# Kernel optimization log

Hardware: AMD Instinct MI355X
Metric: run time of the kernel (lower is better)

The kernel has to match this reference:

```python
import jax, jax.numpy as jnp
import numpy as np
import math

L, D, H = 4, 256, 8
HD = D // H
B, SQ, SK = 2, 1024, 1024
FF = 3 * D
EPS = 1e-5


def setup_inputs() -> dict:
    key = jax.random.key(0)
    ks = jax.random.split(key, 16)
    s = 0.02
    w = lambda k, shape: jax.random.normal(k, shape, jnp.float32) * s
    return {
        "pose": jax.random.normal(ks[0], (B, SQ, D), jnp.float32),
        "vel": jax.random.normal(ks[1], (B, SK, D), jnp.float32),
        "img": jax.random.normal(ks[2], (B, SK, D), jnp.float32),
        "Wq": w(ks[3], (L, D, D)), "bq": jnp.zeros((L, D), jnp.float32),
        "Wk": w(ks[4], (L, D, D)), "bk": jnp.zeros((L, D), jnp.float32),
        "Wv": w(ks[5], (L, D, D)), "bv": jnp.zeros((L, D), jnp.float32),
        "Wo": w(ks[6], (L, D, D)), "bo": jnp.zeros((L, D), jnp.float32),
        "an_g": jnp.ones((L, D), jnp.float32), "an_b": jnp.zeros((L, D), jnp.float32),
        "W1": w(ks[7], (L, D, FF)), "b1": jnp.zeros((L, FF), jnp.float32),
        "W2": w(ks[8], (L, FF, D)), "b2": jnp.zeros((L, D), jnp.float32),
        "fn_g": jnp.ones((L, D), jnp.float32), "fn_b": jnp.zeros((L, D), jnp.float32),
        "n_g": jnp.ones((L, D), jnp.float32), "n_b": jnp.zeros((L, D), jnp.float32),
    }


def entmax15(x):
    # exact alpha=1.5 entmax along the last axis (Peters & Martins 2019)
    x = x * 0.5
    x = x - jnp.max(x, axis=-1, keepdims=True)
    z = -jnp.sort(-x, axis=-1)  # descending
    k = jnp.arange(1, z.shape[-1] + 1, dtype=x.dtype)
    mean = jnp.cumsum(z, axis=-1) / k
    mean_sq = jnp.cumsum(z * z, axis=-1) / k
    ss = k * (mean_sq - mean * mean)
    delta = jnp.clip((1.0 - ss) / k, 0.0)
    tau = mean - jnp.sqrt(delta)
    support = jnp.sum(tau <= z, axis=-1, keepdims=True)  # support size >= 1
    tau_star = jnp.take_along_axis(tau, support - 1, axis=-1)
    p = jnp.clip(x - tau_star, 0.0)
    return p * p


def layer_norm(x, g, b):
    m = jnp.mean(x, axis=-1, keepdims=True)
    v = jnp.mean((x - m) ** 2, axis=-1, keepdims=True)
    return (x - m) * jax.lax.rsqrt(v + EPS) * g + b


def mish(x):
    return x * jnp.tanh(jax.nn.softplus(x))


def reference(pose, vel, img, Wq, bq, Wk, bk, Wv, bv, Wo, bo, an_g, an_b,
              W1, b1, W2, b2, fn_g, fn_b, n_g, n_b):
    def mha(q_in, kv, i):
        bs, sq, _ = q_in.shape
        sk = kv.shape[1]
        q = (q_in @ Wq[i] + bq[i]).reshape(bs, sq, H, HD)
        k = (kv @ Wk[i] + bk[i]).reshape(bs, sk, H, HD)
        v = (kv @ Wv[i] + bv[i]).reshape(bs, sk, H, HD)
        scores = jnp.einsum('bqhd,bkhd->bhqk', q, k) / math.sqrt(HD)
        attn = entmax15(scores)
        out = jnp.einsum('bhqk,bkhd->bqhd', attn, v).reshape(bs, sq, D)
        return out @ Wo[i] + bo[i]

    def cross_layer(x1, x2, i):
        y = layer_norm(mha(x1, x2, i), an_g[i], an_b[i])
        x1 = x1 + y
        y = layer_norm(x1, fn_g[i], fn_b[i])
        h = mish(y @ W1[i] + b1[i]) @ W2[i] + b2[i]
        return x1 + h

    def stack(x, kv):
        for i in range(L):  # small fixed layer loop (shared weights across both paths)
            mem = x
            x = cross_layer(x, kv, i)
            x = layer_norm(x, n_g[i], n_b[i])
            x = x + mem
        return x

    img_out = stack(pose, img)
    pose_out = stack(pose, vel)
    return (pose_out, img_out)
```

## Files before the change

kernel.cpp:

```cpp
#include <hip/hip_runtime.h>
#include <math.h>

#define NL   4
#define DIM  256
#define NH   8
#define HDIM 32
#define SQL  1024
#define SKL  1024
#define FFD  768
#define CB   4
#define ROWS (CB * SQL)

typedef __attribute__((ext_vector_type(8))) short bf16x8;
typedef __attribute__((ext_vector_type(4))) short bf16x4;
typedef __attribute__((ext_vector_type(4))) float f32x4;
typedef __attribute__((ext_vector_type(2))) float f32x2;


__device__ __forceinline__ short f2bf(float f) {
    union { float f; unsigned u; } v; v.f = f;
    unsigned u = v.u + 0x7fffu + ((v.u >> 16) & 1u);
    return (short)(u >> 16);
}

__device__ __forceinline__ float fast_mish(float x) {
    float u = __expf(fminf(x, 20.0f));
    float a = __builtin_fmaf(u, u, 2.0f * u);
    return x * a * __builtin_amdgcn_rcpf(a + 2.0f);
}

__device__ __forceinline__ f32x2 lo2(f32x4 v) { return __builtin_shufflevector(v, v, 0, 1); }
__device__ __forceinline__ f32x2 hi2(f32x4 v) { return __builtin_shufflevector(v, v, 2, 3); }


__global__ __launch_bounds__(256) void init_kernel(
        const float* __restrict__ pose, const float* __restrict__ vel,
        const float* __restrict__ img, float* __restrict__ X,
        short* __restrict__ Xb, short* __restrict__ KVb) {
    int idx = blockIdx.x * 256 + threadIdx.x;
    if (idx >= CB * SQL * DIM) return;
    int c = idx / (SQL * DIM);
    int rem = idx - c * (SQL * DIM);
    int b = c & 1;
    float pv = pose[b * SQL * DIM + rem];
    X[idx]  = pv;
    Xb[idx] = f2bf(pv);
    const float* kv = (c < 2) ? vel : img;
    KVb[idx] = f2bf(kv[b * SQL * DIM + rem]);
}


__global__ __launch_bounds__(256) void transpose_qkvo(
        const float* __restrict__ Wq, const float* __restrict__ Wk,
        const float* __restrict__ Wv, const float* __restrict__ Wo,
        short* __restrict__ Wqt, short* __restrict__ Wkt,
        short* __restrict__ Wvt, short* __restrict__ Wot) {
    __shared__ float tile[64][65];
    int z = blockIdx.z, m = z >> 2, lyr = z & 3;
    const float* src = ((m == 0) ? Wq : (m == 1) ? Wk : (m == 2) ? Wv : Wo)
                       + (size_t)lyr * DIM * DIM;
    short* dst = ((m == 0) ? Wqt : (m == 1) ? Wkt : (m == 2) ? Wvt : Wot)
                 + (size_t)lyr * DIM * DIM;
    int t = threadIdx.x;
    int n0 = blockIdx.x * 64, k0 = blockIdx.y * 64;
#pragma unroll
    for (int i = 0; i < 16; i++) {
        int idx = t + i * 256;
        int r = idx >> 6, c = idx & 63;
        tile[r][c] = src[(size_t)(k0 + r) * DIM + n0 + c];
    }
    __syncthreads();
#pragma unroll
    for (int i = 0; i < 16; i++) {
        int idx = t + i * 256;
        int r = idx >> 6, c = idx & 63;
        dst[(size_t)(n0 + r) * DIM + k0 + c] = f2bf(tile[c][r]);
    }
}

__global__ __launch_bounds__(256) void transpose_w(
        const float* __restrict__ src, short* __restrict__ dst, int K, int N) {
    __shared__ float tile[64][65];
    int t = threadIdx.x;
    int n0 = blockIdx.x * 64, k0 = blockIdx.y * 64;
    const float* s = src + (size_t)blockIdx.z * K * N;
    short* d = dst + (size_t)blockIdx.z * K * N;
#pragma unroll
    for (int i = 0; i < 16; i++) {
        int idx = t + i * 256;
        int r = idx >> 6, c = idx & 63;
        tile[r][c] = s[(size_t)(k0 + r) * N + n0 + c];
    }
    __syncthreads();
#pragma unroll
    for (int i = 0; i < 16; i++) {
        int idx = t + i * 256;
        int r = idx >> 6, c = idx & 63;
        d[(size_t)(n0 + r) * K + k0 + c] = f2bf(tile[c][r]);
    }
}


__global__ __launch_bounds__(256) void qkv_gemm(
        const short* __restrict__ Xb, const short* __restrict__ KVb,
        const short* __restrict__ Wqt, const short* __restrict__ Wkt,
        const short* __restrict__ Wvt,
        const float* __restrict__ bq, const float* __restrict__ bk,
        const float* __restrict__ bv,
        short* __restrict__ Qb, short* __restrict__ Kb, short* __restrict__ Vt,
        float qscale) {
    int z = blockIdx.z;
    const short* A    = (z == 0) ? Xb : KVb;
    const short* Wt   = (z == 0) ? Wqt : (z == 1) ? Wkt : Wvt;
    const float* bias = (z == 0) ? bq : (z == 1) ? bk : bv;
    float scale = (z == 0) ? qscale : 1.0f;

    int t = threadIdx.x, l = t & 63, w = t >> 6;
    int lq = l & 15, lg = l >> 4;
    int bm = blockIdx.y * 64, bn = blockIdx.x * 64;

    const short* ap = A + (size_t)(bm + w * 16 + lq) * DIM + lg * 8;
    const short* wp = Wt + (size_t)(bn + lq) * DIM + lg * 8;

    f32x4 acc[4];
#pragma unroll
    for (int nt = 0; nt < 4; nt++) acc[nt] = (f32x4){0.f, 0.f, 0.f, 0.f};
#pragma unroll
    for (int k0 = 0; k0 < DIM; k0 += 32) {
        bf16x8 af = *(const bf16x8*)(ap + k0);
#pragma unroll
        for (int nt = 0; nt < 4; nt++) {
            bf16x8 bfr = *(const bf16x8*)(wp + (size_t)nt * 16 * DIM + k0);
            acc[nt] = __builtin_amdgcn_mfma_f32_16x16x32_bf16(af, bfr, acc[nt], 0, 0, 0);
        }
    }

    int ms = bm + w * 16 + lg * 4;
#pragma unroll
    for (int nt = 0; nt < 4; nt++) {
        int col = bn + nt * 16 + lq;
        float bv_ = bias[col];
        float v[4];
#pragma unroll
        for (int j = 0; j < 4; j++) v[j] = acc[nt][j] + bv_;
        if (z < 2) {
            short* out = (z == 0) ? Qb : Kb;
#pragma unroll
            for (int j = 0; j < 4; j++) out[(size_t)(ms + j) * DIM + col] = f2bf(v[j] * scale);
        } else {
            int cc = ms >> 10, kl = ms & 1023;
            bf16x4 pk;
#pragma unroll
            for (int j = 0; j < 4; j++) pk[j] = f2bf(v[j]);
            *(bf16x4*)(Vt + ((size_t)(cc * DIM + col)) * SKL + kl) = pk;
        }
    }
}


__global__ __launch_bounds__(256) void gemm_ln2(
        const short* __restrict__ A, const short* __restrict__ Wt,
        const float* __restrict__ bias, const float* __restrict__ Xres,
        const float* __restrict__ ag, const float* __restrict__ ab,
        const float* __restrict__ fg, const float* __restrict__ fb,
        float* __restrict__ x1out, short* __restrict__ yout) {
    __shared__ float gbuf[16][264];
    int t = threadIdx.x, l = t & 63, w = t >> 6;
    int lq = l & 15, lg = l >> 4;
    int bm = blockIdx.x * 16;

    const short* ap = A + (size_t)(bm + lq) * DIM + lg * 8;
    const short* wp = Wt + (size_t)(w * 64 + lq) * DIM + lg * 8;

    f32x4 acc[4];
#pragma unroll
    for (int nt = 0; nt < 4; nt++) acc[nt] = (f32x4){0.f, 0.f, 0.f, 0.f};
#pragma unroll
    for (int k0 = 0; k0 < DIM; k0 += 32) {
        bf16x8 af = *(const bf16x8*)(ap + k0);
#pragma unroll
        for (int nt = 0; nt < 4; nt++) {
            bf16x8 bfr = *(const bf16x8*)(wp + (size_t)nt * 16 * DIM + k0);
            acc[nt] = __builtin_amdgcn_mfma_f32_16x16x32_bf16(af, bfr, acc[nt], 0, 0, 0);
        }
    }
#pragma unroll
    for (int nt = 0; nt < 4; nt++) {
        int col = w * 64 + nt * 16 + lq;
        float bv_ = bias[col];
#pragma unroll
        for (int j = 0; j < 4; j++) gbuf[lg * 4 + j][col] = acc[nt][j] + bv_;
    }
    __syncthreads();

    int g = t >> 4, u = t & 15;
    int row = bm + g;
    float s = 0.f, s2 = 0.f;
#pragma unroll
    for (int i = 0; i < 16; i++) {
        float v = gbuf[g][u + 16 * i];
        s += v; s2 += v * v;
    }
#pragma unroll
    for (int off = 1; off < 16; off <<= 1) { s += __shfl_xor(s, off); s2 += __shfl_xor(s2, off); }
    float m = s * (1.f / DIM);
    float rstd = rsqrtf(s2 * (1.f / DIM) - m * m + 1e-5f);

    float x1v[16];
    float sb = 0.f, sb2 = 0.f;
#pragma unroll
    for (int i = 0; i < 16; i++) {
        int col = u + 16 * i;
        float x1 = Xres[(size_t)row * DIM + col] + (gbuf[g][col] - m) * rstd * ag[col] + ab[col];
        x1v[i] = x1; sb += x1; sb2 += x1 * x1;
    }
#pragma unroll
    for (int off = 1; off < 16; off <<= 1) { sb += __shfl_xor(sb, off); sb2 += __shfl_xor(sb2, off); }
    float m2 = sb * (1.f / DIM);
    float rstd2 = rsqrtf(sb2 * (1.f / DIM) - m2 * m2 + 1e-5f);
#pragma unroll
    for (int i = 0; i < 16; i++) {
        int col = u + 16 * i;
        x1out[(size_t)row * DIM + col] = x1v[i];
        yout[(size_t)row * DIM + col]  = f2bf((x1v[i] - m2) * rstd2 * fg[col] + fb[col]);
    }
}


__global__ __launch_bounds__(256) void gemm_ffn(
        const short* __restrict__ Yb, const short* __restrict__ W1t,
        const float* __restrict__ b1, const short* __restrict__ W2t,
        const float* __restrict__ b2, const float* __restrict__ x1res,
        const float* __restrict__ Xres, const float* __restrict__ g_,
        const float* __restrict__ b_,
        float* __restrict__ outf, short* __restrict__ outb) {
    __shared__ __align__(16) char lds[16 * 776 * 2];
    short (*g1)[776]  = (short(*)[776])lds;
    float (*gbuf)[264] = (float(*)[264])lds;

    int t = threadIdx.x, l = t & 63, w = t >> 6;
    int lq = l & 15, lg = l >> 4;
    int bm = blockIdx.x * 16;

    {
        const short* ap = Yb + (size_t)(bm + lq) * DIM + lg * 8;
        const short* wp = W1t + (size_t)(w * 192 + lq) * DIM + lg * 8;
        f32x4 acc[12];
#pragma unroll
        for (int nt = 0; nt < 12; nt++) acc[nt] = (f32x4){0.f, 0.f, 0.f, 0.f};
#pragma unroll
        for (int k0 = 0; k0 < DIM; k0 += 32) {
            bf16x8 af = *(const bf16x8*)(ap + k0);
#pragma unroll
            for (int nt = 0; nt < 12; nt++) {
                bf16x8 bfr = *(const bf16x8*)(wp + (size_t)nt * 16 * DIM + k0);
                acc[nt] = __builtin_amdgcn_mfma_f32_16x16x32_bf16(af, bfr, acc[nt], 0, 0, 0);
            }
        }
#pragma unroll
        for (int nt = 0; nt < 12; nt++) {
            int col = w * 192 + nt * 16 + lq;
            float bv_ = b1[col];
#pragma unroll
            for (int j = 0; j < 4; j++)
                g1[lg * 4 + j][col] = f2bf(fast_mish(acc[nt][j] + bv_));
        }
    }
    __syncthreads();

    f32x4 acc2[4];
#pragma unroll
    for (int nt = 0; nt < 4; nt++) acc2[nt] = (f32x4){0.f, 0.f, 0.f, 0.f};
    {
        const short* wp2 = W2t + (size_t)(w * 64 + lq) * FFD + lg * 8;
#pragma unroll 6
        for (int ks = 0; ks < 24; ks++) {
            bf16x8 af = *(const bf16x8*)(&g1[lq][ks * 32 + lg * 8]);
#pragma unroll
            for (int nt = 0; nt < 4; nt++) {
                bf16x8 bfr = *(const bf16x8*)(wp2 + (size_t)nt * 16 * FFD + ks * 32);
                acc2[nt] = __builtin_amdgcn_mfma_f32_16x16x32_bf16(af, bfr, acc2[nt], 0, 0, 0);
            }
        }
    }
    __syncthreads();

#pragma unroll
    for (int nt = 0; nt < 4; nt++) {
        int col = w * 64 + nt * 16 + lq;
        float bv_ = b2[col];
#pragma unroll
        for (int j = 0; j < 4; j++) {
            int row = bm + lg * 4 + j;
            gbuf[lg * 4 + j][col] = acc2[nt][j] + bv_ + x1res[(size_t)row * DIM + col];
        }
    }
    __syncthreads();

    int g = t >> 4, u = t & 15;
    int row = bm + g;
    float s = 0.f, s2 = 0.f;
#pragma unroll
    for (int i = 0; i < 16; i++) {
        float v = gbuf[g][u + 16 * i];
        s += v; s2 += v * v;
    }
#pragma unroll
    for (int off = 1; off < 16; off <<= 1) { s += __shfl_xor(s, off); s2 += __shfl_xor(s2, off); }
    float m = s * (1.f / DIM);
    float rstd = rsqrtf(s2 * (1.f / DIM) - m * m + 1e-5f);
#pragma unroll
    for (int i = 0; i < 16; i++) {
        int col = u + 16 * i;
        float o = Xres[(size_t)row * DIM + col] + (gbuf[g][col] - m) * rstd * g_[col] + b_[col];
        outf[(size_t)row * DIM + col] = o;
        if (outb) outb[(size_t)row * DIM + col] = f2bf(o);
    }
}


__global__ __launch_bounds__(256) void attn_mfma(
        const short* __restrict__ Q, const short* __restrict__ K,
        const short* __restrict__ Vt, short* __restrict__ O) {
    int h = blockIdx.y, c = blockIdx.z;
    int qbase = blockIdx.x * 16;
    int t = threadIdx.x, l = t & 63, w = t >> 6;
    int lq = l & 15, lg = l >> 4;

    __shared__ __align__(16) short p_lds[16 * 1024];
    __shared__ float redf[3][4][16];
    float* obuf = (float*)p_lds;

    bf16x8 qfrag = *(const bf16x8*)(Q + ((size_t)(c * SQL + qbase + lq)) * DIM + h * HDIM + lg * 8);

    const int kw = w * 256;
    f32x4 acc[16];
#pragma unroll
    for (int kt = 0; kt < 16; kt++) {
        bf16x8 kf = *(const bf16x8*)(K + ((size_t)(c * SKL + kw + kt * 16 + lq)) * DIM + h * HDIM + lg * 8);
        f32x4 z = {0.f, 0.f, 0.f, 0.f};
        acc[kt] = __builtin_amdgcn_mfma_f32_16x16x32_bf16(kf, qfrag, z, 0, 0, 0);
    }

    const f32x2 z2  = {0.f, 0.f};
    const f32x2 big = {1e30f, 1e30f};
    const f32x2 one = {1.f, 1.f};

    f32x2 mm = lo2(acc[0]);
#pragma unroll
    for (int kt = 0; kt < 16; kt++) {
        mm = __builtin_elementwise_max(mm, lo2(acc[kt]));
        mm = __builtin_elementwise_max(mm, hi2(acc[kt]));
    }
    float m = fmaxf(mm.x, mm.y);
    m = fmaxf(m, __shfl_xor(m, 16));
    m = fmaxf(m, __shfl_xor(m, 32));
    if (l < 16) redf[0][w][l] = m;
    __syncthreads();
    m = fmaxf(fmaxf(redf[0][0][lq], redf[0][1][lq]),
              fmaxf(redf[0][2][lq], redf[0][3][lq]));

    float tau = m - 1.0f;
#pragma unroll 1
    for (int r = 0; r < 5; r++) {
        f32x2 vt = {tau, tau};
        f32x2 S1 = z2, S2 = z2, NN = z2;
#pragma unroll
        for (int kt = 0; kt < 16; kt++) {
            f32x2 y0 = __builtin_elementwise_max(lo2(acc[kt]) - vt, z2);
            f32x2 y1 = __builtin_elementwise_max(hi2(acc[kt]) - vt, z2);
            S1 += y0; S1 += y1;
            S2 += y0 * y0; S2 += y1 * y1;
            NN += __builtin_elementwise_min(y0 * big, one);
            NN += __builtin_elementwise_min(y1 * big, one);
        }
        float sy = S1.x + S1.y, sy2 = S2.x + S2.y, nn = NN.x + NN.y;
        sy  += __shfl_xor(sy, 16);  sy  += __shfl_xor(sy, 32);
        sy2 += __shfl_xor(sy2, 16); sy2 += __shfl_xor(sy2, 32);
        nn  += __shfl_xor(nn, 16);  nn  += __shfl_xor(nn, 32);
        __syncthreads();
        if (l < 16) { redf[0][w][l] = nn; redf[1][w][l] = sy; redf[2][w][l] = sy2; }
        __syncthreads();
        nn  = redf[0][0][lq] + redf[0][1][lq] + redf[0][2][lq] + redf[0][3][lq];
        sy  = redf[1][0][lq] + redf[1][1][lq] + redf[1][2][lq] + redf[1][3][lq];
        sy2 = redf[2][0][lq] + redf[2][1][lq] + redf[2][2][lq] + redf[2][3][lq];
        float disc = fmaxf(sy * sy - nn * (sy2 - 1.0f), 0.f);
        tau = fminf(tau + (sy - sqrtf(disc)) / nn, m - 0.03125f);
    }

    {
        f32x2 vt = {tau, tau};
#pragma unroll
        for (int kt = 0; kt < 16; kt++) {
            f32x2 y0 = __builtin_elementwise_max(lo2(acc[kt]) - vt, z2);
            f32x2 y1 = __builtin_elementwise_max(hi2(acc[kt]) - vt, z2);
            f32x2 p0 = y0 * y0, p1 = y1 * y1;
            unsigned u01, u23;
            asm("v_cvt_pk_bf16_f32 %0, %1, %2" : "=v"(u01) : "v"(p0.x), "v"(p0.y));
            asm("v_cvt_pk_bf16_f32 %0, %1, %2" : "=v"(u23) : "v"(p1.x), "v"(p1.y));
            int k = kw + kt * 16 + lg * 4;
            int byte = lq * 2048 + ((k * 2) ^ (lq << 4));
            *(uint2*)((char*)p_lds + byte) = make_uint2(u01, u23);
        }
    }
    __syncthreads();

    f32x4 o0 = {0.f, 0.f, 0.f, 0.f}, o1 = {0.f, 0.f, 0.f, 0.f};
#pragma unroll
    for (int kt2 = 0; kt2 < 8; kt2++) {
        int k0 = kw + kt2 * 32 + lg * 8;
        int byte = lq * 2048 + ((k0 * 2) ^ (lq << 4));
        bf16x8 pa = *(const bf16x8*)((const char*)p_lds + byte);
        bf16x8 vb0 = *(const bf16x8*)(Vt + ((size_t)(c * DIM + h * HDIM + lq)) * SKL + k0);
        bf16x8 vb1 = *(const bf16x8*)(Vt + ((size_t)(c * DIM + h * HDIM + 16 + lq)) * SKL + k0);
        o0 = __builtin_amdgcn_mfma_f32_16x16x32_bf16(pa, vb0, o0, 0, 0, 0);
        o1 = __builtin_amdgcn_mfma_f32_16x16x32_bf16(pa, vb1, o1, 0, 0, 0);
    }
    __syncthreads();

#pragma unroll
    for (int j = 0; j < 4; j++) {
        obuf[w * 512 + (lg * 4 + j) * 32 + lq]      = o0[j];
        obuf[w * 512 + (lg * 4 + j) * 32 + 16 + lq] = o1[j];
    }
    __syncthreads();
#pragma unroll
    for (int rep = 0; rep < 2; rep++) {
        int e = t + rep * 256;
        int q = e >> 5, d = e & 31;
        float s = obuf[e] + obuf[512 + e] + obuf[1024 + e] + obuf[1536 + e];
        O[((size_t)(c * SQL + qbase + q)) * DIM + h * HDIM + d] = f2bf(s);
    }
}


extern "C" void kernel_launch(void* const* d_in, const int* in_sizes, int n_in,
                              void* d_out, int out_size, void* d_ws, size_t ws_size,
                              hipStream_t stream) {
    const float* pose = (const float*)d_in[0];
    const float* vel  = (const float*)d_in[1];
    const float* img  = (const float*)d_in[2];
    const float* Wq   = (const float*)d_in[3];
    const float* bq   = (const float*)d_in[4];
    const float* Wk   = (const float*)d_in[5];
    const float* bk   = (const float*)d_in[6];
    const float* Wv   = (const float*)d_in[7];
    const float* bv   = (const float*)d_in[8];
    const float* Wo   = (const float*)d_in[9];
    const float* bo   = (const float*)d_in[10];
    const float* an_g = (const float*)d_in[11];
    const float* an_b = (const float*)d_in[12];
    const float* W1   = (const float*)d_in[13];
    const float* b1   = (const float*)d_in[14];
    const float* W2   = (const float*)d_in[15];
    const float* b2   = (const float*)d_in[16];
    const float* fn_g = (const float*)d_in[17];
    const float* fn_b = (const float*)d_in[18];
    const float* n_g  = (const float*)d_in[19];
    const float* n_b  = (const float*)d_in[20];

    const size_t SZ = (size_t)ROWS * DIM;
    float* X    = (float*)d_ws;
    float* X1b  = X + SZ;
    short* Xb   = (short*)(X1b + SZ);
    short* KVb  = Xb + SZ;
    short* T1b  = KVb + SZ;
    short* Qb   = T1b + SZ;
    short* Kb   = Qb + SZ;
    short* Vt   = Kb + SZ;
    short* Yb   = Vt + SZ;
    short* Wqt  = Yb + SZ;
    short* Wkt  = Wqt + (size_t)NL * DIM * DIM;
    short* Wvt  = Wkt + (size_t)NL * DIM * DIM;
    short* Wot  = Wvt + (size_t)NL * DIM * DIM;
    short* W1t  = Wot + (size_t)NL * DIM * DIM;
    short* W2t  = W1t + (size_t)NL * DIM * FFD;

    {
        int total = CB * SQL * DIM;
        init_kernel<<<(total + 255) / 256, 256, 0, stream>>>(pose, vel, img, X, Xb, KVb);
    }
    transpose_qkvo<<<dim3(4, 4, 16), 256, 0, stream>>>(Wq, Wk, Wv, Wo, Wqt, Wkt, Wvt, Wot);
    transpose_w<<<dim3(FFD / 64, DIM / 64, NL), 256, 0, stream>>>(W1, W1t, DIM, FFD);
    transpose_w<<<dim3(DIM / 64, FFD / 64, NL), 256, 0, stream>>>(W2, W2t, FFD, DIM);

    const float qscale = 0.08838834764831845f;

    for (int i = 0; i < NL; i++) {
        const short* Wqt_i = Wqt + (size_t)i * DIM * DIM;
        const short* Wkt_i = Wkt + (size_t)i * DIM * DIM;
        const short* Wvt_i = Wvt + (size_t)i * DIM * DIM;
        const short* Wot_i = Wot + (size_t)i * DIM * DIM;
        const short* W1t_i = W1t + (size_t)i * DIM * FFD;
        const short* W2t_i = W2t + (size_t)i * DIM * FFD;

        qkv_gemm<<<dim3(DIM / 64, ROWS / 64, 3), 256, 0, stream>>>(
            Xb, KVb, Wqt_i, Wkt_i, Wvt_i,
            bq + i * DIM, bk + i * DIM, bv + i * DIM, Qb, Kb, Vt, qscale);

        attn_mfma<<<dim3(SQL / 16, NH, CB), 256, 0, stream>>>(Qb, Kb, Vt, T1b);

        gemm_ln2<<<ROWS / 16, 256, 0, stream>>>(
            T1b, Wot_i, bo + i * DIM, X,
            an_g + i * DIM, an_b + i * DIM, fn_g + i * DIM, fn_b + i * DIM,
            X1b, Yb);

        float* outp  = (i == NL - 1) ? (float*)d_out : X;
        short* outbp = (i == NL - 1) ? nullptr : Xb;
        gemm_ffn<<<ROWS / 16, 256, 0, stream>>>(
            Yb, W1t_i, b1 + i * FFD, W2t_i, b2 + i * DIM, X1b, X,
            n_g + i * DIM, n_b + i * DIM, outp, outbp);
    }

    (void)in_sizes; (void)n_in; (void)out_size; (void)ws_size;
}
```

Before: 457.3 us.

## Merge weight transposes, widen GEMM-LN blocks, early-exit entmax loop, chunk attention PV

```diff
diff --git a/kernel.cpp b/kernel.cpp
--- a/kernel.cpp
+++ b/kernel.cpp
@@ -50,53 +50,44 @@
 }
 
 
-__global__ __launch_bounds__(256) void transpose_qkvo(
+__global__ __launch_bounds__(256) void transpose_all(
         const float* __restrict__ Wq, const float* __restrict__ Wk,
         const float* __restrict__ Wv, const float* __restrict__ Wo,
+        const float* __restrict__ W1, const float* __restrict__ W2,
         short* __restrict__ Wqt, short* __restrict__ Wkt,
-        short* __restrict__ Wvt, short* __restrict__ Wot) {
+        short* __restrict__ Wvt, short* __restrict__ Wot,
+        short* __restrict__ W1t, short* __restrict__ W2t) {
     __shared__ float tile[64][65];
-    int z = blockIdx.z, m = z >> 2, lyr = z & 3;
-    const float* src = ((m == 0) ? Wq : (m == 1) ? Wk : (m == 2) ? Wv : Wo)
-                       + (size_t)lyr * DIM * DIM;
-    short* dst = ((m == 0) ? Wqt : (m == 1) ? Wkt : (m == 2) ? Wvt : Wot)
-                 + (size_t)lyr * DIM * DIM;
+    int z = blockIdx.x;
+    const float* src; short* dst; int K, N, tx, ty;
+    if (z < 256) {
+        int m = z >> 6, lyr = (z >> 4) & 3, r = z & 15;
+        src = ((m == 0) ? Wq : (m == 1) ? Wk : (m == 2) ? Wv : Wo) + (size_t)lyr * DIM * DIM;
+        dst = ((m == 0) ? Wqt : (m == 1) ? Wkt : (m == 2) ? Wvt : Wot) + (size_t)lyr * DIM * DIM;
+        K = DIM; N = DIM; tx = r & 3; ty = r >> 2;
+    } else if (z < 448) {
+        int idx = z - 256, lyr = idx / 48, r = idx % 48;
+        src = W1 + (size_t)lyr * DIM * FFD; dst = W1t + (size_t)lyr * DIM * FFD;
+        K = DIM; N = FFD; tx = r % 12; ty = r / 12;
+    } else {
+        int idx = z - 448, lyr = idx / 48, r = idx % 48;
+        src = W2 + (size_t)lyr * FFD * DIM; dst = W2t + (size_t)lyr * FFD * DIM;
+        K = FFD; N = DIM; tx = r % 4; ty = r / 4;
+    }
     int t = threadIdx.x;
-    int n0 = blockIdx.x * 64, k0 = blockIdx.y * 64;
+    int n0 = tx * 64, k0 = ty * 64;
 #pragma unroll
     for (int i = 0; i < 16; i++) {
         int idx = t + i * 256;
         int r = idx >> 6, c = idx & 63;
-        tile[r][c] = src[(size_t)(k0 + r) * DIM + n0 + c];
+        tile[r][c] = src[(size_t)(k0 + r) * N + n0 + c];
     }
     __syncthreads();
 #pragma unroll
     for (int i = 0; i < 16; i++) {
         int idx = t + i * 256;
         int r = idx >> 6, c = idx & 63;
-        dst[(size_t)(n0 + r) * DIM + k0 + c] = f2bf(tile[c][r]);
-    }
-}
-
-__global__ __launch_bounds__(256) void transpose_w(
-        const float* __restrict__ src, short* __restrict__ dst, int K, int N) {
-    __shared__ float tile[64][65];
-    int t = threadIdx.x;
-    int n0 = blockIdx.x * 64, k0 = blockIdx.y * 64;
-    const float* s = src + (size_t)blockIdx.z * K * N;
-    short* d = dst + (size_t)blockIdx.z * K * N;
-#pragma unroll
-    for (int i = 0; i < 16; i++) {
-        int idx = t + i * 256;
-        int r = idx >> 6, c = idx & 63;
-        tile[r][c] = s[(size_t)(k0 + r) * N + n0 + c];
-    }
-    __syncthreads();
-#pragma unroll
-    for (int i = 0; i < 16; i++) {
-        int idx = t + i * 256;
-        int r = idx >> 6, c = idx & 63;
-        d[(size_t)(n0 + r) * K + k0 + c] = f2bf(tile[c][r]);
+        dst[(size_t)(n0 + r) * K + k0 + c] = f2bf(tile[c][r]);
     }
 }
 
@@ -158,7 +149,7 @@
 }
 
 
-__global__ __launch_bounds__(256) void gemm_ln2(
+__global__ __launch_bounds__(512) void gemm_ln2(
         const short* __restrict__ A, const short* __restrict__ Wt,
         const float* __restrict__ bias, const float* __restrict__ Xres,
         const float* __restrict__ ag, const float* __restrict__ ab,
@@ -170,64 +161,64 @@
     int bm = blockIdx.x * 16;
 
     const short* ap = A + (size_t)(bm + lq) * DIM + lg * 8;
-    const short* wp = Wt + (size_t)(w * 64 + lq) * DIM + lg * 8;
-
-    f32x4 acc[4];
-#pragma unroll
-    for (int nt = 0; nt < 4; nt++) acc[nt] = (f32x4){0.f, 0.f, 0.f, 0.f};
+    const short* wp = Wt + (size_t)(w * 32 + lq) * DIM + lg * 8;
+
+    f32x4 acc[2];
+    acc[0] = (f32x4){0.f, 0.f, 0.f, 0.f};
+    acc[1] = (f32x4){0.f, 0.f, 0.f, 0.f};
 #pragma unroll
     for (int k0 = 0; k0 < DIM; k0 += 32) {
         bf16x8 af = *(const bf16x8*)(ap + k0);
 #pragma unroll
-        for (int nt = 0; nt < 4; nt++) {
+        for (int nt = 0; nt < 2; nt++) {
             bf16x8 bfr = *(const bf16x8*)(wp + (size_t)nt * 16 * DIM + k0);
             acc[nt] = __builtin_amdgcn_mfma_f32_16x16x32_bf16(af, bfr, acc[nt], 0, 0, 0);
         }
     }
 #pragma unroll
-    for (int nt = 0; nt < 4; nt++) {
-        int col = w * 64 + nt * 16 + lq;
+    for (int nt = 0; nt < 2; nt++) {
+        int col = w * 32 + nt * 16 + lq;
         float bv_ = bias[col];
 #pragma unroll
         for (int j = 0; j < 4; j++) gbuf[lg * 4 + j][col] = acc[nt][j] + bv_;
     }
     __syncthreads();
 
-    int g = t >> 4, u = t & 15;
+    int g = t >> 5, u = t & 31;
     int row = bm + g;
     float s = 0.f, s2 = 0.f;
 #pragma unroll
-    for (int i = 0; i < 16; i++) {
-        float v = gbuf[g][u + 16 * i];
+    for (int i = 0; i < 8; i++) {
+        float v = gbuf[g][u + 32 * i];
         s += v; s2 += v * v;
     }
 #pragma unroll
-    for (int off = 1; off < 16; off <<= 1) { s += __shfl_xor(s, off); s2 += __shfl_xor(s2, off); }
+    for (int off = 1; off < 32; off <<= 1) { s += __shfl_xor(s, off); s2 += __shfl_xor(s2, off); }
     float m = s * (1.f / DIM);
     float rstd = rsqrtf(s2 * (1.f / DIM) - m * m + 1e-5f);
 
-    float x1v[16];
+    float x1v[8];
     float sb = 0.f, sb2 = 0.f;
 #pragma unroll
-    for (int i = 0; i < 16; i++) {
-        int col = u + 16 * i;
+    for (int i = 0; i < 8; i++) {
+        int col = u + 32 * i;
         float x1 = Xres[(size_t)row * DIM + col] + (gbuf[g][col] - m) * rstd * ag[col] + ab[col];
         x1v[i] = x1; sb += x1; sb2 += x1 * x1;
     }
 #pragma unroll
-    for (int off = 1; off < 16; off <<= 1) { sb += __shfl_xor(sb, off); sb2 += __shfl_xor(sb2, off); }
+    for (int off = 1; off < 32; off <<= 1) { sb += __shfl_xor(sb, off); sb2 += __shfl_xor(sb2, off); }
     float m2 = sb * (1.f / DIM);
     float rstd2 = rsqrtf(sb2 * (1.f / DIM) - m2 * m2 + 1e-5f);
 #pragma unroll
-    for (int i = 0; i < 16; i++) {
-        int col = u + 16 * i;
+    for (int i = 0; i < 8; i++) {
+        int col = u + 32 * i;
         x1out[(size_t)row * DIM + col] = x1v[i];
         yout[(size_t)row * DIM + col]  = f2bf((x1v[i] - m2) * rstd2 * fg[col] + fb[col]);
     }
 }
 
 
-__global__ __launch_bounds__(256) void gemm_ffn(
+__global__ __launch_bounds__(512) void gemm_ffn(
         const short* __restrict__ Yb, const short* __restrict__ W1t,
         const float* __restrict__ b1, const short* __restrict__ W2t,
         const float* __restrict__ b2, const float* __restrict__ x1res,
@@ -235,7 +226,7 @@
         const float* __restrict__ b_,
         float* __restrict__ outf, short* __restrict__ outb) {
     __shared__ __align__(16) char lds[16 * 776 * 2];
-    short (*g1)[776]  = (short(*)[776])lds;
+    short (*g1)[776]   = (short(*)[776])lds;
     float (*gbuf)[264] = (float(*)[264])lds;
 
     int t = threadIdx.x, l = t & 63, w = t >> 6;
@@ -244,22 +235,22 @@
 
     {
         const short* ap = Yb + (size_t)(bm + lq) * DIM + lg * 8;
-        const short* wp = W1t + (size_t)(w * 192 + lq) * DIM + lg * 8;
-        f32x4 acc[12];
-#pragma unroll
-        for (int nt = 0; nt < 12; nt++) acc[nt] = (f32x4){0.f, 0.f, 0.f, 0.f};
+        const short* wp = W1t + (size_t)(w * 96 + lq) * DIM + lg * 8;
+        f32x4 acc[6];
+#pragma unroll
+        for (int nt = 0; nt < 6; nt++) acc[nt] = (f32x4){0.f, 0.f, 0.f, 0.f};
 #pragma unroll
         for (int k0 = 0; k0 < DIM; k0 += 32) {
             bf16x8 af = *(const bf16x8*)(ap + k0);
 #pragma unroll
-            for (int nt = 0; nt < 12; nt++) {
+            for (int nt = 0; nt < 6; nt++) {
                 bf16x8 bfr = *(const bf16x8*)(wp + (size_t)nt * 16 * DIM + k0);
                 acc[nt] = __builtin_amdgcn_mfma_f32_16x16x32_bf16(af, bfr, acc[nt], 0, 0, 0);
             }
         }
 #pragma unroll
-        for (int nt = 0; nt < 12; nt++) {
-            int col = w * 192 + nt * 16 + lq;
+        for (int nt = 0; nt < 6; nt++) {
+            int col = w * 96 + nt * 16 + lq;
             float bv_ = b1[col];
 #pragma unroll
             for (int j = 0; j < 4; j++)
@@ -268,16 +259,16 @@
     }
     __syncthreads();
 
-    f32x4 acc2[4];
-#pragma unroll
-    for (int nt = 0; nt < 4; nt++) acc2[nt] = (f32x4){0.f, 0.f, 0.f, 0.f};
+    f32x4 acc2[2];
+    acc2[0] = (f32x4){0.f, 0.f, 0.f, 0.f};
+    acc2[1] = (f32x4){0.f, 0.f, 0.f, 0.f};
     {
-        const short* wp2 = W2t + (size_t)(w * 64 + lq) * FFD + lg * 8;
+        const short* wp2 = W2t + (size_t)(w * 32 + lq) * FFD + lg * 8;
 #pragma unroll 6
         for (int ks = 0; ks < 24; ks++) {
             bf16x8 af = *(const bf16x8*)(&g1[lq][ks * 32 + lg * 8]);
 #pragma unroll
-            for (int nt = 0; nt < 4; nt++) {
+            for (int nt = 0; nt < 2; nt++) {
                 bf16x8 bfr = *(const bf16x8*)(wp2 + (size_t)nt * 16 * FFD + ks * 32);
                 acc2[nt] = __builtin_amdgcn_mfma_f32_16x16x32_bf16(af, bfr, acc2[nt], 0, 0, 0);
             }
@@ -286,8 +277,8 @@
     __syncthreads();
 
 #pragma unroll
-    for (int nt = 0; nt < 4; nt++) {
-        int col = w * 64 + nt * 16 + lq;
+    for (int nt = 0; nt < 2; nt++) {
+        int col = w * 32 + nt * 16 + lq;
         float bv_ = b2[col];
 #pragma unroll
         for (int j = 0; j < 4; j++) {
@@ -297,21 +288,21 @@
     }
     __syncthreads();
 
-    int g = t >> 4, u = t & 15;
+    int g = t >> 5, u = t & 31;
     int row = bm + g;
     float s = 0.f, s2 = 0.f;
 #pragma unroll
-    for (int i = 0; i < 16; i++) {
-        float v = gbuf[g][u + 16 * i];
+    for (int i = 0; i < 8; i++) {
+        float v = gbuf[g][u + 32 * i];
         s += v; s2 += v * v;
     }
 #pragma unroll
-    for (int off = 1; off < 16; off <<= 1) { s += __shfl_xor(s, off); s2 += __shfl_xor(s2, off); }
+    for (int off = 1; off < 32; off <<= 1) { s += __shfl_xor(s, off); s2 += __shfl_xor(s2, off); }
     float m = s * (1.f / DIM);
     float rstd = rsqrtf(s2 * (1.f / DIM) - m * m + 1e-5f);
 #pragma unroll
-    for (int i = 0; i < 16; i++) {
-        int col = u + 16 * i;
+    for (int i = 0; i < 8; i++) {
+        int col = u + 32 * i;
         float o = Xres[(size_t)row * DIM + col] + (gbuf[g][col] - m) * rstd * g_[col] + b_[col];
         outf[(size_t)row * DIM + col] = o;
         if (outb) outb[(size_t)row * DIM + col] = f2bf(o);
@@ -327,9 +318,9 @@
     int t = threadIdx.x, l = t & 63, w = t >> 6;
     int lq = l & 15, lg = l >> 4;
 
-    __shared__ __align__(16) short p_lds[16 * 1024];
-    __shared__ float redf[3][4][16];
-    float* obuf = (float*)p_lds;
+    __shared__ __align__(16) short p_lds[4][1024];
+    __shared__ float obuf[4][512];
+    __shared__ float redf[2][3][4][16];
 
     bf16x8 qfrag = *(const bf16x8*)(Q + ((size_t)(c * SQL + qbase + lq)) * DIM + h * HDIM + lg * 8);
 
@@ -355,14 +346,14 @@
     float m = fmaxf(mm.x, mm.y);
     m = fmaxf(m, __shfl_xor(m, 16));
     m = fmaxf(m, __shfl_xor(m, 32));
-    if (l < 16) redf[0][w][l] = m;
-    __syncthreads();
-    m = fmaxf(fmaxf(redf[0][0][lq], redf[0][1][lq]),
-              fmaxf(redf[0][2][lq], redf[0][3][lq]));
+    if (l < 16) redf[1][0][w][l] = m;
+    __syncthreads();
+    m = fmaxf(fmaxf(redf[1][0][0][lq], redf[1][0][1][lq]),
+              fmaxf(redf[1][0][2][lq], redf[1][0][3][lq]));
 
     float tau = m - 1.0f;
-#pragma unroll 1
-    for (int r = 0; r < 5; r++) {
+    int r = 0;
+    for (;;) {
         f32x2 vt = {tau, tau};
         f32x2 S1 = z2, S2 = z2, NN = z2;
 #pragma unroll
@@ -378,57 +369,65 @@
         sy  += __shfl_xor(sy, 16);  sy  += __shfl_xor(sy, 32);
         sy2 += __shfl_xor(sy2, 16); sy2 += __shfl_xor(sy2, 32);
         nn  += __shfl_xor(nn, 16);  nn  += __shfl_xor(nn, 32);
+        int b = r & 1;
+        if (l < 16) { redf[b][0][w][l] = nn; redf[b][1][w][l] = sy; redf[b][2][w][l] = sy2; }
         __syncthreads();
-        if (l < 16) { redf[0][w][l] = nn; redf[1][w][l] = sy; redf[2][w][l] = sy2; }
-        __syncthreads();
-        nn  = redf[0][0][lq] + redf[0][1][lq] + redf[0][2][lq] + redf[0][3][lq];
-        sy  = redf[1][0][lq] + redf[1][1][lq] + redf[1][2][lq] + redf[1][3][lq];
-        sy2 = redf[2][0][lq] + redf[2][1][lq] + redf[2][2][lq] + redf[2][3][lq];
+        nn  = redf[b][0][0][lq] + redf[b][0][1][lq] + redf[b][0][2][lq] + redf[b][0][3][lq];
+        sy  = redf[b][1][0][lq] + redf[b][1][1][lq] + redf[b][1][2][lq] + redf[b][1][3][lq];
+        sy2 = redf[b][2][0][lq] + redf[b][2][1][lq] + redf[b][2][2][lq] + redf[b][2][3][lq];
         float disc = fmaxf(sy * sy - nn * (sy2 - 1.0f), 0.f);
-        tau = fminf(tau + (sy - sqrtf(disc)) / nn, m - 0.03125f);
-    }
-
+        float delta = (sy - sqrtf(disc)) / nn;
+        tau = fminf(tau + delta, m - 0.03125f);
+        r++;
+        if (r >= 6 || __all(delta < 1e-6f)) break;
+    }
+
+    f32x4 o0 = {0.f, 0.f, 0.f, 0.f}, o1 = {0.f, 0.f, 0.f, 0.f};
+    const short* vbase0 = Vt + ((size_t)(c * DIM + h * HDIM + lq)) * SKL;
+    const short* vbase1 = vbase0 + (size_t)16 * SKL;
     {
         f32x2 vt = {tau, tau};
-#pragma unroll
-        for (int kt = 0; kt < 16; kt++) {
-            f32x2 y0 = __builtin_elementwise_max(lo2(acc[kt]) - vt, z2);
-            f32x2 y1 = __builtin_elementwise_max(hi2(acc[kt]) - vt, z2);
-            f32x2 p0 = y0 * y0, p1 = y1 * y1;
-            unsigned u01, u23;
-            asm("v_cvt_pk_bf16_f32 %0, %1, %2" : "=v"(u01) : "v"(p0.x), "v"(p0.y));
-            asm("v_cvt_pk_bf16_f32 %0, %1, %2" : "=v"(u23) : "v"(p1.x), "v"(p1.y));
-            int k = kw + kt * 16 + lg * 4;
-            int byte = lq * 2048 + ((k * 2) ^ (lq << 4));
-            *(uint2*)((char*)p_lds + byte) = make_uint2(u01, u23);
-        }
-    }
-    __syncthreads();
-
-    f32x4 o0 = {0.f, 0.f, 0.f, 0.f}, o1 = {0.f, 0.f, 0.f, 0.f};
-#pragma unroll
-    for (int kt2 = 0; kt2 < 8; kt2++) {
-        int k0 = kw + kt2 * 32 + lg * 8;
-        int byte = lq * 2048 + ((k0 * 2) ^ (lq << 4));
-        bf16x8 pa = *(const bf16x8*)((const char*)p_lds + byte);
-        bf16x8 vb0 = *(const bf16x8*)(Vt + ((size_t)(c * DIM + h * HDIM + lq)) * SKL + k0);
-        bf16x8 vb1 = *(const bf16x8*)(Vt + ((size_t)(c * DIM + h * HDIM + 16 + lq)) * SKL + k0);
-        o0 = __builtin_amdgcn_mfma_f32_16x16x32_bf16(pa, vb0, o0, 0, 0, 0);
-        o1 = __builtin_amdgcn_mfma_f32_16x16x32_bf16(pa, vb1, o1, 0, 0, 0);
-    }
-    __syncthreads();
+        int swz = (lq & 7) << 4;
+#pragma unroll
+        for (int c2 = 0; c2 < 4; c2++) {
+#pragma unroll
+            for (int k4 = 0; k4 < 4; k4++) {
+                int kt = c2 * 4 + k4;
+                f32x2 y0 = __builtin_elementwise_max(lo2(acc[kt]) - vt, z2);
+                f32x2 y1 = __builtin_elementwise_max(hi2(acc[kt]) - vt, z2);
+                f32x2 p0 = y0 * y0, p1 = y1 * y1;
+                unsigned u01, u23;
+                asm("v_cvt_pk_bf16_f32 %0, %1, %2" : "=v"(u01) : "v"(p0.x), "v"(p0.y));
+                asm("v_cvt_pk_bf16_f32 %0, %1, %2" : "=v"(u23) : "v"(p1.x), "v"(p1.y));
+                int klocal = k4 * 16 + lg * 4;
+                int byte = lq * 128 + ((klocal * 2) ^ swz);
+                *(uint2*)((char*)p_lds[w] + byte) = make_uint2(u01, u23);
+            }
+#pragma unroll
+            for (int k2 = 0; k2 < 2; k2++) {
+                int klocal0 = k2 * 32 + lg * 8;
+                int byte = lq * 128 + ((klocal0 * 2) ^ swz);
+                bf16x8 pa = *(const bf16x8*)((const char*)p_lds[w] + byte);
+                int k0 = kw + c2 * 64 + klocal0;
+                bf16x8 vb0 = *(const bf16x8*)(vbase0 + k0);
+                bf16x8 vb1 = *(const bf16x8*)(vbase1 + k0);
+                o0 = __builtin_amdgcn_mfma_f32_16x16x32_bf16(pa, vb0, o0, 0, 0, 0);
+                o1 = __builtin_amdgcn_mfma_f32_16x16x32_bf16(pa, vb1, o1, 0, 0, 0);
+            }
+        }
+    }
 
 #pragma unroll
     for (int j = 0; j < 4; j++) {
-        obuf[w * 512 + (lg * 4 + j) * 32 + lq]      = o0[j];
-        obuf[w * 512 + (lg * 4 + j) * 32 + 16 + lq] = o1[j];
+        obuf[w][(lg * 4 + j) * 32 + lq]      = o0[j];
+        obuf[w][(lg * 4 + j) * 32 + 16 + lq] = o1[j];
     }
     __syncthreads();
 #pragma unroll
     for (int rep = 0; rep < 2; rep++) {
         int e = t + rep * 256;
         int q = e >> 5, d = e & 31;
-        float s = obuf[e] + obuf[512 + e] + obuf[1024 + e] + obuf[1536 + e];
+        float s = obuf[0][e] + obuf[1][e] + obuf[2][e] + obuf[3][e];
         O[((size_t)(c * SQL + qbase + q)) * DIM + h * HDIM + d] = f2bf(s);
     }
 }
@@ -480,9 +479,8 @@
         int total = CB * SQL * DIM;
         init_kernel<<<(total + 255) / 256, 256, 0, stream>>>(pose, vel, img, X, Xb, KVb);
     }
-    transpose_qkvo<<<dim3(4, 4, 16), 256, 0, stream>>>(Wq, Wk, Wv, Wo, Wqt, Wkt, Wvt, Wot);
-    transpose_w<<<dim3(FFD / 64, DIM / 64, NL), 256, 0, stream>>>(W1, W1t, DIM, FFD);
-    transpose_w<<<dim3(DIM / 64, FFD / 64, NL), 256, 0, stream>>>(W2, W2t, FFD, DIM);
+    transpose_all<<<640, 256, 0, stream>>>(Wq, Wk, Wv, Wo, W1, W2,
+                                           Wqt, Wkt, Wvt, Wot, W1t, W2t);
 
     const float qscale = 0.08838834764831845f;
 
@@ -500,14 +498,14 @@
 
         attn_mfma<<<dim3(SQL / 16, NH, CB), 256, 0, stream>>>(Qb, Kb, Vt, T1b);
 
-        gemm_ln2<<<ROWS / 16, 256, 0, stream>>>(
+        gemm_ln2<<<ROWS / 16, 512, 0, stream>>>(
             T1b, Wot_i, bo + i * DIM, X,
             an_g + i * DIM, an_b + i * DIM, fn_g + i * DIM, fn_b + i * DIM,
             X1b, Yb);
 
         float* outp  = (i == NL - 1) ? (float*)d_out : X;
         short* outbp = (i == NL - 1) ? nullptr : Xb;
-        gemm_ffn<<<ROWS / 16, 256, 0, stream>>>(
+        gemm_ffn<<<ROWS / 16, 512, 0, stream>>>(
             Yb, W1t_i, b1 + i * FFD, W2t_i, b2 + i * DIM, X1b, X,
             n_g + i * DIM, n_b + i * DIM, outp, outbp);
     }
```

Result: faster. 415.2 us (-9.2%).
